# Optimization experiments

Hardware: AMD Instinct MI355X
Metric: run time of the kernel (lower is better)

## Reference

```python
import jax, jax.numpy as jnp
import numpy as np

D_MODEL = 768
N_HEADS = 12
HEAD_DIM = D_MODEL // N_HEADS
NEG = -10000.0


def setup_inputs() -> dict:
    key = jax.random.key(0)
    ks = jax.random.split(key, 8)
    B, S, D = 2, 2048, D_MODEL
    inp = {
        "q": jax.random.normal(ks[0], (B, S, D), dtype=jnp.float32),
        "k": jax.random.normal(ks[1], (B, S, D), dtype=jnp.float32),
        "v": jax.random.normal(ks[2], (B, S, D), dtype=jnp.float32),
        "attn_mask": jax.random.randint(ks[3], (B, S), 0, 2, dtype=jnp.int32),
        # weights stored [in, out]; apply as x @ W (equivalent to torch Linear)
        "Wq": jax.random.normal(ks[4], (D, D), dtype=jnp.float32) / np.sqrt(D),
        "Wk": jax.random.normal(ks[5], (D, D), dtype=jnp.float32) / np.sqrt(D),
        "Wv": jax.random.normal(ks[6], (D, D), dtype=jnp.float32) / np.sqrt(D),
        "Wo": jax.random.normal(ks[7], (D, D), dtype=jnp.float32) / np.sqrt(D),
        "mask_future": 1,
    }
    return inp


def reference(q, k, v, attn_mask, Wq, Wk, Wv, Wo, mask_future):
    B, S, D = q.shape
    H, hd = N_HEADS, HEAD_DIM
    # project and split heads -> [B, H, S, hd]
    qh = (q @ Wq).reshape(B, S, H, hd).transpose(0, 2, 1, 3)
    kh = (k @ Wk).reshape(B, S, H, hd).transpose(0, 2, 1, 3)
    vh = (v @ Wv).reshape(B, S, H, hd).transpose(0, 2, 1, 3)

    scale = 1.0 / np.sqrt(hd).astype(np.float32)
    # full [B, H, L, S] score matrix (naive SDPA, as in the original)
    scores = jnp.einsum("bhld,bhsd->bhls", qh, kh) * scale
    if mask_future:
        causal = jnp.triu(jnp.full((S, S), NEG, dtype=scores.dtype), k=1)
        scores = scores + causal
    # padding mask: [B, S] -> broadcast over heads and query positions
    pad = attn_mask[:, None, None, :] == 0
    scores = jnp.where(pad, NEG, scores)
    attn = jax.nn.softmax(scores, axis=-1)  # dropout p=0.0 -> identity
    out = jnp.einsum("bhls,bhsd->bhld", attn, vh)  # [B, H, L, hd]
    out = out.transpose(0, 2, 1, 3).reshape(B, S, D)
    return out @ Wo
```

## Files before the change

### kernel.cpp

```cpp
#include <hip/hip_runtime.h>


#define NEGV (-10000.0f)

typedef __attribute__((ext_vector_type(8))) short v8s;
typedef __attribute__((ext_vector_type(4))) float v4f;
typedef __attribute__((ext_vector_type(8))) unsigned short v8u;
typedef __fp16 h2v __attribute__((ext_vector_type(2)));

#define GLDS16(g, l)                                            \
  __builtin_amdgcn_global_load_lds(                             \
      (const __attribute__((address_space(1))) void*)(g),       \
      (__attribute__((address_space(3))) void*)(l), 16, 0, 0)

__device__ __forceinline__ unsigned short f2bf(float f) {
  unsigned int u = __float_as_uint(f);
  u += 0x7FFFu + ((u >> 16) & 1u);
  return (unsigned short)(u >> 16);
}

__device__ __forceinline__ int pkmax_f16(int a, int b) {
  int r;
  asm("v_pk_max_f16 %0, %1, %2" : "=v"(r) : "v"(a), "v"(b));
  return r;
}

__global__ __launch_bounds__(256) void transpose_w(
    const float* __restrict__ w0, const float* __restrict__ w1,
    const float* __restrict__ w2, const float* __restrict__ w3,
    unsigned short* __restrict__ t0, unsigned short* __restrict__ t1,
    unsigned short* __restrict__ t2, unsigned short* __restrict__ t3) {
  const float* w; unsigned short* t;
  switch (blockIdx.z) {
    case 0: w = w0; t = t0; break;
    case 1: w = w1; t = t1; break;
    case 2: w = w2; t = t2; break;
    default: w = w3; t = t3; break;
  }
  __shared__ unsigned short tile[32][33];
  const int tx = threadIdx.x & 31, ty = threadIdx.x >> 5;
  const int x0 = blockIdx.x * 32, y0 = blockIdx.y * 32;
#pragma unroll
  for (int j = 0; j < 4; j++)
    tile[ty + j * 8][tx] = f2bf(w[(size_t)(y0 + ty + j * 8) * 768 + x0 + tx]);
  __syncthreads();
#pragma unroll
  for (int j = 0; j < 4; j++)
    t[(size_t)(x0 + ty + j * 8) * 768 + y0 + tx] = tile[tx][ty + j * 8];
}

template <bool ABF16HEAD, int CMODE>
__device__ __forceinline__ void gemm_core(const void* __restrict__ A,
                                          const unsigned short* __restrict__ Wt,
                                          void* __restrict__ C) {
  const int tid = threadIdx.x;
  const int wave = tid >> 6, lane = tid & 63;
  const int quad = lane >> 4, l16 = lane & 15;
  const int wm = wave >> 1, wn = wave & 1;
  const int bm = blockIdx.x * 128, bn = blockIdx.y * 128;

  __shared__ __align__(16) unsigned short As[128 * 32];
  __shared__ __align__(16) unsigned short Bs[128 * 32];

  v4f acc[4][4];
#pragma unroll
  for (int i = 0; i < 4; i++)
#pragma unroll
    for (int j = 0; j < 4; j++) acc[i][j] = (v4f){0.f, 0.f, 0.f, 0.f};

  for (int kt = 0; kt < 24; kt++) {
    __syncthreads();
#pragma unroll
    for (int p = 0; p < 2; p++) {
      int idx = p * 256 + tid;
      int r = idx >> 2, c0 = (idx & 3) << 3;
      int rg = bm + r, c = kt * 32 + c0;
      if (ABF16HEAD) {
        size_t aoff = ((size_t)((rg >> 11) * 12 + (c >> 6)) * 2048 +
                       (rg & 2047)) * 64 + (c & 63);
        GLDS16((const unsigned short*)A + aoff,
               &As[(size_t)(p * 256 + wave * 64) * 8]);
      } else {
        const float* Af = (const float*)A;
        size_t aoff = (size_t)rg * 768 + c;
        float4 x0 = *(const float4*)(Af + aoff);
        float4 x1 = *(const float4*)(Af + aoff + 4);
        v8u tmp;
        tmp[0] = f2bf(x0.x); tmp[1] = f2bf(x0.y);
        tmp[2] = f2bf(x0.z); tmp[3] = f2bf(x0.w);
        tmp[4] = f2bf(x1.x); tmp[5] = f2bf(x1.y);
        tmp[6] = f2bf(x1.z); tmp[7] = f2bf(x1.w);
        *(uint4*)&As[r * 32 + c0] = *(uint4*)&tmp;
      }
      GLDS16(&Wt[(size_t)(bn + r) * 768 + c],
             &Bs[(size_t)(p * 256 + wave * 64) * 8]);
    }
    __syncthreads();

    v8s aF[4], bF[4];
#pragma unroll
    for (int mt = 0; mt < 4; mt++)
      aF[mt] = *(const v8s*)&As[(wm * 64 + mt * 16 + l16) * 32 + quad * 8];
#pragma unroll
    for (int nt = 0; nt < 4; nt++)
      bF[nt] = *(const v8s*)&Bs[(wn * 64 + nt * 16 + l16) * 32 + quad * 8];
#pragma unroll
    for (int mt = 0; mt < 4; mt++)
#pragma unroll
      for (int nt = 0; nt < 4; nt++)
        acc[mt][nt] = __builtin_amdgcn_mfma_f32_16x16x32_bf16(
            aF[mt], bF[nt], acc[mt][nt], 0, 0, 0);
  }

#pragma unroll
  for (int mt = 0; mt < 4; mt++) {
#pragma unroll
    for (int i = 0; i < 4; i++) {
      int row = bm + wm * 64 + mt * 16 + quad * 4 + i;
#pragma unroll
      for (int nt = 0; nt < 4; nt++) {
        int col = bn + wn * 64 + nt * 16 + l16;
        if (CMODE == 1) {
          ((float*)C)[(size_t)row * 768 + col] = acc[mt][nt][i];
        } else if (CMODE == 0) {
          size_t off = ((size_t)((row >> 11) * 12 + (col >> 6)) * 2048 +
                        (row & 2047)) * 64 + (col & 63);
          ((unsigned short*)C)[off] = f2bf(acc[mt][nt][i]);
        } else {
          size_t off = (size_t)((row >> 11) * 12 + (col >> 6)) * (64 * 2048) +
                       (size_t)(col & 63) * 2048 + (row & 2047);
          ((unsigned short*)C)[off] = f2bf(acc[mt][nt][i]);
        }
      }
    }
  }
}

__global__ __launch_bounds__(256) void gemm_qkv(
    const float* __restrict__ xq, const float* __restrict__ xk,
    const float* __restrict__ xv, const unsigned short* __restrict__ wqt,
    const unsigned short* __restrict__ wkt, const unsigned short* __restrict__ wvt,
    unsigned short* __restrict__ qh, unsigned short* __restrict__ kh,
    unsigned short* __restrict__ vht) {
  if (blockIdx.z == 2) {
    gemm_core<false, 2>((const void*)xv, wvt, (void*)vht);
  } else if (blockIdx.z == 1) {
    gemm_core<false, 0>((const void*)xk, wkt, (void*)kh);
  } else {
    gemm_core<false, 0>((const void*)xq, wqt, (void*)qh);
  }
}

__global__ __launch_bounds__(256) void gemm_o(
    const unsigned short* __restrict__ oat, const unsigned short* __restrict__ wot,
    float* __restrict__ out) {
  gemm_core<true, 1>((const void*)oat, wot, (void*)out);
}

__global__ __launch_bounds__(256) void attn_kernel(
    const unsigned short* __restrict__ qh, const unsigned short* __restrict__ kh,
    const unsigned short* __restrict__ vht, const int* __restrict__ attn_mask,
    const int* __restrict__ mask_future, unsigned short* __restrict__ o) {
  const int S = 2048, HD = 64, NH = 12;

  const int nlin = blockIdx.x + 32 * blockIdx.y;
  const int m_ = nlin & 255, t_ = nlin >> 8;
  const int i_ = (t_ == 1) ? (511 - m_) : (t_ * 256 + m_);
  const int qt = 31 - i_ / 24;
  const int bh = i_ - (i_ / 24) * 24;
  const int b = bh / NH, h = bh % NH;

  const int tid = threadIdx.x;
  const int wave = tid >> 6, lane = tid & 63;
  const int quad = lane >> 4, l16 = lane & 15;

  __shared__ __align__(16) unsigned short Ks[2][64 * 72];
  __shared__ __align__(16) unsigned short Vt[2][64 * 72];
  __shared__ __align__(16) unsigned short Ps[4][16 * 72];
  __shared__ int Ms[2][64];
  __shared__ int s_flag;

  const size_t head_off = (size_t)(b * NH + h) * S * HD;
  const unsigned short* Kb = kh + head_off;
  const unsigned short* Vb = vht + head_off;

  const int mf = mask_future[0];
  if (tid == 0) s_flag = 0;

  const int qrowA = qt * 64 + wave * 16 + l16;
  v8s aQ[2];
  {
    const unsigned short* qp = qh + head_off + (size_t)qrowA * HD + quad * 8;
    aQ[0] = *(const v8s*)(qp);
    aQ[1] = *(const v8s*)(qp + 32);
  }
  const int qbase = qt * 64 + wave * 16 + quad * 4;

  float m_i[4];
  v4f accO[4], accL;
#pragma unroll
  for (int i = 0; i < 4; i++) m_i[i] = -1e30f;
  accL = (v4f){0.f, 0.f, 0.f, 0.f};
#pragma unroll
  for (int dt = 0; dt < 4; dt++) accO[dt] = (v4f){0.f, 0.f, 0.f, 0.f};

  v8s ones;
#pragma unroll
  for (int j = 0; j < 8; j++) ones[j] = (short)0x3F80;

  const int kt_causal = mf ? qt : (S / 64 - 1);
  const int r0 = tid >> 3, c0s = (tid & 7) << 3;

  auto nexttile = [&](int t) -> int {
    if (t < kt_causal) return t + 1;
    if (t == kt_causal) return (mf && kt_causal < S / 64 - 1) ? t + 1 : -1;
    return (t < S / 64 - 1) ? t + 1 : -1;
  };

  uint4 pk0, pk1, pv0, pv1;
  int pm = 0;
  int rtile = -1, stile = -1;

  auto prefetch = [&](int kt) {
    const uint4* srck = (const uint4*)(Kb + (size_t)kt * 64 * HD);
    pk0 = srck[tid];
    pk1 = srck[256 + tid];
    const unsigned short* vp = Vb + (size_t)r0 * S + kt * 64 + c0s;
    pv0 = *(const uint4*)vp;
    pv1 = *(const uint4*)(vp + (size_t)32 * S);
    if (tid < 64) pm = attn_mask[b * S + kt * 64 + tid];
    rtile = kt;
  };

  auto stage = [&](int kb) {
    *(uint4*)&Ks[kb][r0 * 72 + c0s] = pk0;
    *(uint4*)&Ks[kb][(r0 + 32) * 72 + c0s] = pk1;
    *(uint4*)&Vt[kb][r0 * 72 + c0s] = pv0;
    *(uint4*)&Vt[kb][(r0 + 32) * 72 + c0s] = pv1;
    if (tid < 64) Ms[kb][tid] = pm;
  };

  for (int phase = 0; phase < 2; phase++) {
    int kt_lo, kt_hi;
    if (phase == 0) { kt_lo = 0; kt_hi = kt_causal; }
    else {
      bool need = (m_i[0] < -5000.f) || (m_i[1] < -5000.f) ||
                  (m_i[2] < -5000.f) || (m_i[3] < -5000.f);
      if (need) s_flag = 1;
      __syncthreads();
      if (!s_flag) break;
      kt_lo = kt_causal + 1; kt_hi = S / 64 - 1;
      if (kt_lo > kt_hi) break;
    }

    if (stile != kt_lo) {
      if (rtile != kt_lo) prefetch(kt_lo);
      stage(kt_lo & 1);
      stile = kt_lo;
      int nx = nexttile(kt_lo);
      if (nx >= 0) prefetch(nx);
    }

    for (int kt = kt_lo; kt <= kt_hi; kt++) {
      __syncthreads();

      int nkt = nexttile(kt);
      if (nkt >= 0 && stile != nkt) {
        stage(nkt & 1);
        stile = nkt;
        int n2 = nexttile(nkt);
        if (n2 >= 0) prefetch(n2);
      }

      const int kb = kt & 1;
      const unsigned short* KsB = Ks[kb];
      const unsigned short* VtB = Vt[kb];
      const int* MsB = Ms[kb];

      v4f sc[4];
      __builtin_amdgcn_s_setprio(1);
#pragma unroll
      for (int nt = 0; nt < 4; nt++) {
        const unsigned short* kp = &KsB[(nt * 16 + l16) * 72 + quad * 8];
        v8s b0 = *(const v8s*)kp;
        v8s b1 = *(const v8s*)(kp + 32);
        v4f z = (v4f){0.f, 0.f, 0.f, 0.f};
        z = __builtin_amdgcn_mfma_f32_16x16x32_bf16(aQ[0], b0, z, 0, 0, 0);
        z = __builtin_amdgcn_mfma_f32_16x16x32_bf16(aQ[1], b1, z, 0, 0, 0);
        sc[nt] = z;
      }
      __builtin_amdgcn_s_setprio(0);

#pragma unroll
      for (int nt = 0; nt < 4; nt++) {
        int key = kt * 64 + nt * 16 + l16;
        bool pad = (MsB[nt * 16 + l16] == 0);
#pragma unroll
        for (int i = 0; i < 4; i++) {
          float v = sc[nt][i] * 0.125f;
          v += (mf && (key > qbase + i)) ? NEGV : 0.f;
          v = pad ? NEGV : v;
          sc[nt][i] = v;
        }
      }

      float m4[4];
#pragma unroll
      for (int i = 0; i < 4; i++)
        m4[i] = fmaxf(fmaxf(sc[0][i], sc[1][i]), fmaxf(sc[2][i], sc[3][i]));
      union { h2v h; int v; } pk01, pk23;
      pk01.h = __builtin_amdgcn_cvt_pkrtz(m4[0], m4[1]);
      pk23.h = __builtin_amdgcn_cvt_pkrtz(m4[2], m4[3]);
      int v01 = pk01.v, v23 = pk23.v;
#pragma unroll
      for (int mk = 1; mk <= 8; mk <<= 1) {
        v01 = pkmax_f16(v01, __shfl_xor(v01, mk));
        v23 = pkmax_f16(v23, __shfl_xor(v23, mk));
      }
      union { int v; h2v h; } u01, u23;
      u01.v = v01; u23.v = v23;
      float mx[4] = {(float)u01.h[0], (float)u01.h[1],
                     (float)u23.h[0], (float)u23.h[1]};

#pragma unroll
      for (int i = 0; i < 4; i++) {
        float mnew = fmaxf(m_i[i], mx[i]);
        float alpha = __expf(m_i[i] - mnew);
        m_i[i] = mnew;
#pragma unroll
        for (int nt = 0; nt < 4; nt++)
          sc[nt][i] = __expf(sc[nt][i] - mnew);
#pragma unroll
        for (int dt = 0; dt < 4; dt++) accO[dt][i] *= alpha;
        accL[i] *= alpha;
      }

#pragma unroll
      for (int nt = 0; nt < 4; nt++)
#pragma unroll
        for (int i = 0; i < 4; i++)
          Ps[wave][(quad * 4 + i) * 72 + nt * 16 + l16] = f2bf(sc[nt][i]);

      __builtin_amdgcn_s_setprio(1);
#pragma unroll
      for (int ks = 0; ks < 2; ks++) {
        v8s aP = *(const v8s*)&Ps[wave][l16 * 72 + ks * 32 + quad * 8];
        accL = __builtin_amdgcn_mfma_f32_16x16x32_bf16(aP, ones, accL, 0, 0, 0);
#pragma unroll
        for (int dt = 0; dt < 4; dt++) {
          v8s bV = *(const v8s*)&VtB[(dt * 16 + l16) * 72 + ks * 32 + quad * 8];
          accO[dt] =
              __builtin_amdgcn_mfma_f32_16x16x32_bf16(aP, bV, accO[dt], 0, 0, 0);
        }
      }
      __builtin_amdgcn_s_setprio(0);
    }
    if (phase == 0) __syncthreads();
  }

#pragma unroll
  for (int i = 0; i < 4; i++) {
    float inv = 1.f / accL[i];
    int qr = qbase + i;
    size_t base = head_off + (size_t)qr * HD;
#pragma unroll
    for (int dt = 0; dt < 4; dt++)
      o[base + dt * 16 + l16] = f2bf(accO[dt][i] * inv);
  }
}

extern "C" void kernel_launch(void* const* d_in, const int* in_sizes, int n_in,
                              void* d_out, int out_size, void* d_ws, size_t ws_size,
                              hipStream_t stream) {
  const float* q  = (const float*)d_in[0];
  const float* k  = (const float*)d_in[1];
  const float* v  = (const float*)d_in[2];
  const int* amask = (const int*)d_in[3];
  const float* Wq = (const float*)d_in[4];
  const float* Wk = (const float*)d_in[5];
  const float* Wv = (const float*)d_in[6];
  const float* Wo = (const float*)d_in[7];
  const int* mf  = (const int*)d_in[8];
  float* out = (float*)d_out;

  unsigned short* ws = (unsigned short*)d_ws;
  unsigned short* qh = ws;
  unsigned short* kh = qh + 3145728;
  unsigned short* vh = kh + 3145728;
  unsigned short* wqt = vh + 3145728;
  unsigned short* wkt = wqt + 589824;
  unsigned short* wvt = wkt + 589824;
  unsigned short* wot = wvt + 589824;
  unsigned short* vht = (unsigned short*)d_out;

  transpose_w<<<dim3(24, 24, 4), 256, 0, stream>>>(Wq, Wk, Wv, Wo,
                                                   wqt, wkt, wvt, wot);
  gemm_qkv<<<dim3(32, 6, 3), 256, 0, stream>>>(q, k, v, wqt, wkt, wvt,
                                               qh, kh, vht);
  attn_kernel<<<dim3(32, 24), 256, 0, stream>>>(qh, kh, vht, amask, mf, qh);
  gemm_o<<<dim3(32, 6), 256, 0, stream>>>(qh, wot, out);
}
```

Measured before the change: 237.3 us.

## Transpose score MFMA, use lazy softmax rescale and ballot padding mask

Swaps the MFMA operands in the QK^T product so each lane holds one query row across keys. This lets the row max be reduced with two shuffles, where the old code needed a packed fp16 shuffle tree. Adds a lazy rescale that skips the alpha multiply on the accumulators when the running max grows by no more than 8. It also packs P into bf16 pairs with v_cvt_pk_bf16_f32 and stores them as 8-byte writes. The padding mask now lives in a per-wave ballot bitmask instead of shared memory. The V-transposed GEMM epilogue is replaced by a row-major store plus a separate transpose kernel. That adds an extra launch and a round trip of V through memory, and the lazy rescale adds some numerical risk.

```diff
diff --git a/kernel.cpp b/kernel.cpp
--- a/kernel.cpp
+++ b/kernel.cpp
@@ -6,7 +6,6 @@
 typedef __attribute__((ext_vector_type(8))) short v8s;
 typedef __attribute__((ext_vector_type(4))) float v4f;
 typedef __attribute__((ext_vector_type(8))) unsigned short v8u;
-typedef __fp16 h2v __attribute__((ext_vector_type(2)));
 
 #define GLDS16(g, l)                                            \
   __builtin_amdgcn_global_load_lds(                             \
@@ -19,9 +18,9 @@
   return (unsigned short)(u >> 16);
 }
 
-__device__ __forceinline__ int pkmax_f16(int a, int b) {
-  int r;
-  asm("v_pk_max_f16 %0, %1, %2" : "=v"(r) : "v"(a), "v"(b));
+__device__ __forceinline__ unsigned int cvt_pk_bf16(float lo, float hi) {
+  unsigned int r;
+  asm("v_cvt_pk_bf16_f32 %0, %1, %2" : "=v"(r) : "v"(lo), "v"(hi));
   return r;
 }
 
@@ -49,7 +48,24 @@
     t[(size_t)(x0 + ty + j * 8) * 768 + y0 + tx] = tile[tx][ty + j * 8];
 }
 
-template <bool ABF16HEAD, int CMODE>
+__global__ __launch_bounds__(256) void transpose_vh(
+    const unsigned short* __restrict__ vh, unsigned short* __restrict__ vht) {
+  __shared__ unsigned short tile[32][33];
+  const size_t hoff = (size_t)blockIdx.z * 2048 * 64;
+  const unsigned short* src = vh + hoff;
+  unsigned short* dst = vht + hoff;
+  const int s0 = blockIdx.x * 32, d0 = blockIdx.y * 32;
+  const int tx = threadIdx.x & 31, ty = threadIdx.x >> 5;
+#pragma unroll
+  for (int j = 0; j < 4; j++)
+    tile[ty + j * 8][tx] = src[(size_t)(s0 + ty + j * 8) * 64 + d0 + tx];
+  __syncthreads();
+#pragma unroll
+  for (int j = 0; j < 4; j++)
+    dst[(size_t)(d0 + ty + j * 8) * 2048 + s0 + tx] = tile[tx][ty + j * 8];
+}
+
+template <bool ABF16HEAD, bool CF32ROW>
 __device__ __forceinline__ void gemm_core(const void* __restrict__ A,
                                           const unsigned short* __restrict__ Wt,
                                           void* __restrict__ C) {
@@ -120,15 +136,11 @@
 #pragma unroll
       for (int nt = 0; nt < 4; nt++) {
         int col = bn + wn * 64 + nt * 16 + l16;
-        if (CMODE == 1) {
+        if (CF32ROW) {
           ((float*)C)[(size_t)row * 768 + col] = acc[mt][nt][i];
-        } else if (CMODE == 0) {
+        } else {
           size_t off = ((size_t)((row >> 11) * 12 + (col >> 6)) * 2048 +
                         (row & 2047)) * 64 + (col & 63);
-          ((unsigned short*)C)[off] = f2bf(acc[mt][nt][i]);
-        } else {
-          size_t off = (size_t)((row >> 11) * 12 + (col >> 6)) * (64 * 2048) +
-                       (size_t)(col & 63) * 2048 + (row & 2047);
           ((unsigned short*)C)[off] = f2bf(acc[mt][nt][i]);
         }
       }
@@ -141,20 +153,20 @@
     const float* __restrict__ xv, const unsigned short* __restrict__ wqt,
     const unsigned short* __restrict__ wkt, const unsigned short* __restrict__ wvt,
     unsigned short* __restrict__ qh, unsigned short* __restrict__ kh,
-    unsigned short* __restrict__ vht) {
-  if (blockIdx.z == 2) {
-    gemm_core<false, 2>((const void*)xv, wvt, (void*)vht);
-  } else if (blockIdx.z == 1) {
-    gemm_core<false, 0>((const void*)xk, wkt, (void*)kh);
-  } else {
-    gemm_core<false, 0>((const void*)xq, wqt, (void*)qh);
-  }
+    unsigned short* __restrict__ vh) {
+  const float* A; const unsigned short* Wt; unsigned short* C;
+  switch (blockIdx.z) {
+    case 0: A = xq; Wt = wqt; C = qh; break;
+    case 1: A = xk; Wt = wkt; C = kh; break;
+    default: A = xv; Wt = wvt; C = vh; break;
+  }
+  gemm_core<false, false>((const void*)A, Wt, (void*)C);
 }
 
 __global__ __launch_bounds__(256) void gemm_o(
     const unsigned short* __restrict__ oat, const unsigned short* __restrict__ wot,
     float* __restrict__ out) {
-  gemm_core<true, 1>((const void*)oat, wot, (void*)out);
+  gemm_core<true, true>((const void*)oat, wot, (void*)out);
 }
 
 __global__ __launch_bounds__(256) void attn_kernel(
@@ -177,7 +189,6 @@
   __shared__ __align__(16) unsigned short Ks[2][64 * 72];
   __shared__ __align__(16) unsigned short Vt[2][64 * 72];
   __shared__ __align__(16) unsigned short Ps[4][16 * 72];
-  __shared__ int Ms[2][64];
   __shared__ int s_flag;
 
   const size_t head_off = (size_t)(b * NH + h) * S * HD;
@@ -187,19 +198,17 @@
   const int mf = mask_future[0];
   if (tid == 0) s_flag = 0;
 
-  const int qrowA = qt * 64 + wave * 16 + l16;
+  const int qrow_l = qt * 64 + wave * 16 + l16;
   v8s aQ[2];
   {
-    const unsigned short* qp = qh + head_off + (size_t)qrowA * HD + quad * 8;
+    const unsigned short* qp = qh + head_off + (size_t)qrow_l * HD + quad * 8;
     aQ[0] = *(const v8s*)(qp);
     aQ[1] = *(const v8s*)(qp + 32);
   }
-  const int qbase = qt * 64 + wave * 16 + quad * 4;
-
-  float m_i[4];
+  const int qbase_D = qt * 64 + wave * 16 + quad * 4;
+
+  float m_i = -1e30f;
   v4f accO[4], accL;
-#pragma unroll
-  for (int i = 0; i < 4; i++) m_i[i] = -1e30f;
   accL = (v4f){0.f, 0.f, 0.f, 0.f};
 #pragma unroll
   for (int dt = 0; dt < 4; dt++) accO[dt] = (v4f){0.f, 0.f, 0.f, 0.f};
@@ -218,7 +227,8 @@
   };
 
   uint4 pk0, pk1, pv0, pv1;
-  int pm = 0;
+  int pmv = 0;
+  unsigned long long msk0 = 0, msk1 = 0;
   int rtile = -1, stile = -1;
 
   auto prefetch = [&](int kt) {
@@ -228,7 +238,7 @@
     const unsigned short* vp = Vb + (size_t)r0 * S + kt * 64 + c0s;
     pv0 = *(const uint4*)vp;
     pv1 = *(const uint4*)(vp + (size_t)32 * S);
-    if (tid < 64) pm = attn_mask[b * S + kt * 64 + tid];
+    pmv = attn_mask[b * S + kt * 64 + lane];
     rtile = kt;
   };
 
@@ -237,16 +247,15 @@
     *(uint4*)&Ks[kb][(r0 + 32) * 72 + c0s] = pk1;
     *(uint4*)&Vt[kb][r0 * 72 + c0s] = pv0;
     *(uint4*)&Vt[kb][(r0 + 32) * 72 + c0s] = pv1;
-    if (tid < 64) Ms[kb][tid] = pm;
+    unsigned long long mk = __ballot(pmv != 0);
+    if (kb) msk1 = mk; else msk0 = mk;
   };
 
   for (int phase = 0; phase < 2; phase++) {
     int kt_lo, kt_hi;
     if (phase == 0) { kt_lo = 0; kt_hi = kt_causal; }
     else {
-      bool need = (m_i[0] < -5000.f) || (m_i[1] < -5000.f) ||
-                  (m_i[2] < -5000.f) || (m_i[3] < -5000.f);
-      if (need) s_flag = 1;
+      if (m_i < -5000.f) s_flag = 1;
       __syncthreads();
       if (!s_flag) break;
       kt_lo = kt_causal + 1; kt_hi = S / 64 - 1;
@@ -275,71 +284,72 @@
       const int kb = kt & 1;
       const unsigned short* KsB = Ks[kb];
       const unsigned short* VtB = Vt[kb];
-      const int* MsB = Ms[kb];
+      const unsigned long long mk = kb ? msk1 : msk0;
 
       v4f sc[4];
       __builtin_amdgcn_s_setprio(1);
 #pragma unroll
       for (int nt = 0; nt < 4; nt++) {
         const unsigned short* kp = &KsB[(nt * 16 + l16) * 72 + quad * 8];
-        v8s b0 = *(const v8s*)kp;
-        v8s b1 = *(const v8s*)(kp + 32);
+        v8s k0 = *(const v8s*)kp;
+        v8s k1 = *(const v8s*)(kp + 32);
         v4f z = (v4f){0.f, 0.f, 0.f, 0.f};
-        z = __builtin_amdgcn_mfma_f32_16x16x32_bf16(aQ[0], b0, z, 0, 0, 0);
-        z = __builtin_amdgcn_mfma_f32_16x16x32_bf16(aQ[1], b1, z, 0, 0, 0);
+        z = __builtin_amdgcn_mfma_f32_16x16x32_bf16(k0, aQ[0], z, 0, 0, 0);
+        z = __builtin_amdgcn_mfma_f32_16x16x32_bf16(k1, aQ[1], z, 0, 0, 0);
         sc[nt] = z;
       }
       __builtin_amdgcn_s_setprio(0);
 
 #pragma unroll
       for (int nt = 0; nt < 4; nt++) {
-        int key = kt * 64 + nt * 16 + l16;
-        bool pad = (MsB[nt * 16 + l16] == 0);
 #pragma unroll
         for (int i = 0; i < 4; i++) {
+          int kid = nt * 16 + quad * 4 + i;
+          int key = kt * 64 + kid;
           float v = sc[nt][i] * 0.125f;
-          v += (mf && (key > qbase + i)) ? NEGV : 0.f;
-          v = pad ? NEGV : v;
+          v += (mf && (key > qrow_l)) ? NEGV : 0.f;
+          v = ((mk >> kid) & 1ull) ? v : NEGV;
           sc[nt][i] = v;
         }
       }
 
-      float m4[4];
-#pragma unroll
-      for (int i = 0; i < 4; i++)
-        m4[i] = fmaxf(fmaxf(sc[0][i], sc[1][i]), fmaxf(sc[2][i], sc[3][i]));
-      union { h2v h; int v; } pk01, pk23;
-      pk01.h = __builtin_amdgcn_cvt_pkrtz(m4[0], m4[1]);
-      pk23.h = __builtin_amdgcn_cvt_pkrtz(m4[2], m4[3]);
-      int v01 = pk01.v, v23 = pk23.v;
-#pragma unroll
-      for (int mk = 1; mk <= 8; mk <<= 1) {
-        v01 = pkmax_f16(v01, __shfl_xor(v01, mk));
-        v23 = pkmax_f16(v23, __shfl_xor(v23, mk));
-      }
-      union { int v; h2v h; } u01, u23;
-      u01.v = v01; u23.v = v23;
-      float mx[4] = {(float)u01.h[0], (float)u01.h[1],
-                     (float)u23.h[0], (float)u23.h[1]};
-
-#pragma unroll
-      for (int i = 0; i < 4; i++) {
-        float mnew = fmaxf(m_i[i], mx[i]);
-        float alpha = __expf(m_i[i] - mnew);
-        m_i[i] = mnew;
-#pragma unroll
-        for (int nt = 0; nt < 4; nt++)
-          sc[nt][i] = __expf(sc[nt][i] - mnew);
-#pragma unroll
-        for (int dt = 0; dt < 4; dt++) accO[dt][i] *= alpha;
-        accL[i] *= alpha;
-      }
-
-#pragma unroll
-      for (int nt = 0; nt < 4; nt++)
+      float mx;
+      {
+        float a = fmaxf(fmaxf(sc[0][0], sc[0][1]), fmaxf(sc[0][2], sc[0][3]));
+        float b2 = fmaxf(fmaxf(sc[1][0], sc[1][1]), fmaxf(sc[1][2], sc[1][3]));
+        float c = fmaxf(fmaxf(sc[2][0], sc[2][1]), fmaxf(sc[2][2], sc[2][3]));
+        float d = fmaxf(fmaxf(sc[3][0], sc[3][1]), fmaxf(sc[3][2], sc[3][3]));
+        mx = fmaxf(fmaxf(a, b2), fmaxf(c, d));
+      }
+      mx = fmaxf(mx, __shfl_xor(mx, 16));
+      mx = fmaxf(mx, __shfl_xor(mx, 32));
+
+      if (!__all(mx - m_i <= 8.0f)) {
+        float mnew = fmaxf(m_i, mx);
+        float alpha = __expf(m_i - mnew);
+        m_i = mnew;
+        float a0 = __shfl(alpha, quad * 4 + 0);
+        float a1 = __shfl(alpha, quad * 4 + 1);
+        float a2 = __shfl(alpha, quad * 4 + 2);
+        float a3 = __shfl(alpha, quad * 4 + 3);
+#pragma unroll
+        for (int dt = 0; dt < 4; dt++) {
+          accO[dt][0] *= a0; accO[dt][1] *= a1;
+          accO[dt][2] *= a2; accO[dt][3] *= a3;
+        }
+        accL[0] *= a0; accL[1] *= a1; accL[2] *= a2; accL[3] *= a3;
+      }
+
+#pragma unroll
+      for (int nt = 0; nt < 4; nt++) {
 #pragma unroll
         for (int i = 0; i < 4; i++)
-          Ps[wave][(quad * 4 + i) * 72 + nt * 16 + l16] = f2bf(sc[nt][i]);
+          sc[nt][i] = __expf(sc[nt][i] - m_i);
+        uint2 w;
+        w.x = cvt_pk_bf16(sc[nt][0], sc[nt][1]);
+        w.y = cvt_pk_bf16(sc[nt][2], sc[nt][3]);
+        *(uint2*)&Ps[wave][l16 * 72 + nt * 16 + quad * 4] = w;
+      }
 
       __builtin_amdgcn_s_setprio(1);
 #pragma unroll
@@ -361,7 +371,7 @@
 #pragma unroll
   for (int i = 0; i < 4; i++) {
     float inv = 1.f / accL[i];
-    int qr = qbase + i;
+    int qr = qbase_D + i;
     size_t base = head_off + (size_t)qr * HD;
 #pragma unroll
     for (int dt = 0; dt < 4; dt++)
@@ -396,7 +406,8 @@
   transpose_w<<<dim3(24, 24, 4), 256, 0, stream>>>(Wq, Wk, Wv, Wo,
                                                    wqt, wkt, wvt, wot);
   gemm_qkv<<<dim3(32, 6, 3), 256, 0, stream>>>(q, k, v, wqt, wkt, wvt,
-                                               qh, kh, vht);
+                                               qh, kh, vh);
+  transpose_vh<<<dim3(64, 2, 24), 256, 0, stream>>>(vh, vht);
   attn_kernel<<<dim3(32, 24), 256, 0, stream>>>(qh, kh, vht, amask, mf, qh);
   gemm_o<<<dim3(32, 6), 256, 0, stream>>>(qh, wot, out);
 }
```

After: 212.9 us. 1.11x faster.
